# Performance work log

Measured on AMD Instinct MI355X. Metric: run time of the kernel, lower is better.

The kernel has to match this reference:

```python
import jax, jax.numpy as jnp
import numpy as np

N, C_IN, HF, WF = 4, 256, 128, 128
IMG_H, IMG_W = 1024, 1024
A = 3  # anchors per location (1 size x 3 aspect ratios), matches RPNHead
OBJ_THR, IOU_THR = 0.3, 0.7
PRE_NMS, POST_NMS = 2000, 300  # pre-NMS top-k (== top_k_proposals_training), post-NMS top-k (testing)


def setup_inputs() -> dict:
    key = jax.random.key(0)
    ks = jax.random.split(key, 5)
    return {
        "feat": jax.random.normal(ks[0], (N, C_IN, HF, WF), jnp.float32),
        "conv_w": jax.random.normal(ks[1], (256, C_IN, 3, 3), jnp.float32) * 0.02,
        "conv_b": jnp.zeros((256,), jnp.float32),
        "det_w": jax.random.normal(ks[2], (A, 256, 1, 1), jnp.float32) * 0.05,
        "det_b": jnp.zeros((A,), jnp.float32),
        "reg_w": jax.random.normal(ks[3], (4 * A, 256, 1, 1), jnp.float32) * 0.02,
        "reg_b": jnp.zeros((4 * A,), jnp.float32),
    }


def _conv(x, w, b, pad):
    y = jax.lax.conv_general_dilated(x, w, (1, 1), [(pad, pad), (pad, pad)],
                                     dimension_numbers=("NCHW", "OIHW", "NCHW"))
    return y + b[None, :, None, None]


def _anchors():
    # AnchorGenerator.generate_anchors + grid_anchors, stride = image // grid
    scales = jnp.array([128.0], jnp.float32)
    ratios = jnp.array([0.5, 1.0, 2.0], jnp.float32)
    hr = jnp.sqrt(ratios)
    wr = 1.0 / hr
    ws = (wr[:, None] * scales[None, :]).reshape(-1)
    hs = (hr[:, None] * scales[None, :]).reshape(-1)
    base = jnp.round(jnp.stack([-ws, -hs, ws, hs], axis=1) / 2.0)  # [A,4]
    sx = jnp.arange(WF, dtype=jnp.float32) * (IMG_W // WF)
    sy = jnp.arange(HF, dtype=jnp.float32) * (IMG_H // HF)
    yy, xx = jnp.meshgrid(sy, sx, indexing="ij")
    shifts = jnp.stack([xx.ravel(), yy.ravel(), xx.ravel(), yy.ravel()], axis=1)  # [H*W,4]
    return (shifts[:, None, :] + base[None, :, :]).reshape(-1, 4)  # [H*W*A,4]


def _decode(anchors, deltas):
    # Faithful to source, including the x/y swap in the anchor-center computation.
    x1, y1, x2, y2 = anchors[..., 0], anchors[..., 1], anchors[..., 2], anchors[..., 3]
    aw = x2 - x1
    ah = y2 - y1
    acx = y1 + aw / 2  # (sic) matches original code
    acy = x1 + ah / 2  # (sic)
    dx, dy, dw, dh = deltas[..., 0], deltas[..., 1], deltas[..., 2], deltas[..., 3]
    px = acx + dx * aw
    py = acy + dy * ah
    pw = aw * jnp.exp(dw)
    ph = ah * jnp.exp(dh)
    return jnp.stack([px - pw / 2, py - ph / 2, px + pw / 2, py + ph / 2], axis=-1)


def _filter_one(boxes, scores):
    # clip -> degenerate filter -> objectness threshold -> NMS -> top-k, fixed shapes
    w = boxes[:, 2] - boxes[:, 0]
    h = boxes[:, 3] - boxes[:, 1]
    valid = (scores > OBJ_THR) & (w > 0) & (h > 0)
    s = jnp.where(valid, scores, -jnp.inf)
    top_s, top_i = jax.lax.top_k(s, PRE_NMS)
    b = boxes[top_i]
    v = valid[top_i]
    area = jnp.maximum(b[:, 2] - b[:, 0], 0) * jnp.maximum(b[:, 3] - b[:, 1], 0)
    ix1 = jnp.maximum(b[:, None, 0], b[None, :, 0])
    iy1 = jnp.maximum(b[:, None, 1], b[None, :, 1])
    ix2 = jnp.minimum(b[:, None, 2], b[None, :, 2])
    iy2 = jnp.minimum(b[:, None, 3], b[None, :, 3])
    inter = jnp.maximum(ix2 - ix1, 0) * jnp.maximum(iy2 - iy1, 0)
    iou = inter / jnp.maximum(area[:, None] + area[None, :] - inter, 1e-9)
    idxs = jnp.arange(PRE_NMS)

    def body(keep, i):
        sup = jnp.any((iou[i] > IOU_THR) & keep & (idxs < i))
        return keep.at[i].set(v[i] & ~sup), None

    keep, _ = jax.lax.scan(body, jnp.zeros(PRE_NMS, bool), idxs)
    fs = jnp.where(keep, top_s, -jnp.inf)
    sel_s, sel_i = jax.lax.top_k(fs, POST_NMS)
    kept = keep[sel_i]
    out = jnp.concatenate([b[sel_i], sel_s[:, None]], axis=-1)  # [POST,5] = box + score
    return jnp.where(kept[:, None], out, 0.0)


def reference(feat, conv_w, conv_b, det_w, det_b, reg_w, reg_b):
    x = _conv(feat, conv_w, conv_b, 1)                      # fpn conv 3x3, no activation
    obj = jax.nn.sigmoid(_conv(x, det_w, det_b, 0)).reshape(N, -1)  # [N, A*H*W]
    d = _conv(x, reg_w, reg_b, 0)                           # [N, 4A, H, W]
    d = d.reshape(N, 4, A, HF, WF).transpose(0, 2, 3, 4, 1).reshape(N, -1, 4)
    anchors = _anchors()                                    # [A_total, 4]
    props = _decode(anchors[None], d)
    props = jnp.stack([
        jnp.clip(props[..., 0], 0, IMG_W), jnp.clip(props[..., 1], 0, IMG_H),
        jnp.clip(props[..., 2], 0, IMG_W), jnp.clip(props[..., 3], 0, IMG_H)], axis=-1)
    return jax.vmap(_filter_one)(props, obj)  # [N, POST_NMS, 5]
```

## Files before the change

kernel.cpp:

```cpp
#include <hip/hip_runtime.h>
#include <hip/hip_bf16.h>
#include <hip/hip_fp16.h>
#include <stdint.h>
#include <math.h>

#define N_IMG 4
#define CIN 256
#define HFD 128
#define WFD 128
#define HW (HFD*WFD)
#define NA 3
#define NPROP (NA*HW)
#define PRE_NMS 2000
#define POST_NMS 300

__device__ __forceinline__ unsigned long long rl64(unsigned long long v, int i) {
    unsigned int lo = (unsigned int)__builtin_amdgcn_readlane((int)(unsigned int)v, i);
    unsigned int hi = (unsigned int)__builtin_amdgcn_readlane((int)(unsigned int)(v >> 32), i);
    return ((unsigned long long)hi << 32) | (unsigned long long)lo;
}

__device__ __forceinline__ double sum4(const double* __restrict__ PART, size_t cp) {
    const size_t S = (size_t)1 << 20;
    return (PART[cp] + PART[cp + S]) + (PART[cp + 2 * S] + PART[cp + 3 * S]);
}

__device__ __forceinline__ void decode_box(int i, double dx, double dy, double dwv, double dhv,
                                           double& c1o, double& c2o, double& c3o, double& c4o) {
    int loc = i / 3, aa = i % 3;
    int hh = loc >> 7, wwi = loc & 127;
    double sx = (double)(wwi * 8), sy = (double)(hh * 8);
    double bx1 = (aa == 0) ? -91.0 : (aa == 1 ? -64.0 : -45.0);
    double by1 = (aa == 0) ? -45.0 : (aa == 1 ? -64.0 : -91.0);
    double x1 = sx + bx1, y1 = sy + by1, x2 = sx - bx1, y2 = sy - by1;
    double aw = x2 - x1, ahh = y2 - y1;
    double acx = y1 + aw * 0.5;
    double acy = x1 + ahh * 0.5;
    double px = acx + dx * aw, py = acy + dy * ahh;
    double pw = aw * exp(dwv), ph = ahh * exp(dhv);
    double c1 = px - pw * 0.5, c2 = py - ph * 0.5, c3 = px + pw * 0.5, c4 = py + ph * 0.5;
    c1o = fmin(fmax(c1, 0.0), 1024.0);
    c2o = fmin(fmax(c2, 0.0), 1024.0);
    c3o = fmin(fmax(c3, 0.0), 1024.0);
    c4o = fmin(fmax(c4, 0.0), 1024.0);
}

__global__ __launch_bounds__(256) void k_effw64(const float* __restrict__ cw, const float* __restrict__ cb,
                                                const float* __restrict__ dw_, const float* __restrict__ db_,
                                                const float* __restrict__ rw_, const float* __restrict__ rb_,
                                                double* __restrict__ E64, double* __restrict__ EB64,
                                                unsigned long long* __restrict__ PSPREF,
                                                int* __restrict__ PSNEED,
                                                uint32_t* __restrict__ HIST,
                                                uint32_t* __restrict__ CNT)
{
    int b = blockIdx.x;
    int tid = threadIdx.x;
    if (b < 144) {
        __shared__ float hwl[15][260];
        __shared__ float wt[256][16];
        int k0 = b * 16;
        for (int idx = tid; idx < 15 * 256; idx += 256) {
            int c = idx >> 8, co = idx & 255;
            hwl[c][co] = (c < 3) ? dw_[c * 256 + co] : rw_[(c - 3) * 256 + co];
        }
        for (int idx = tid; idx < 4096; idx += 256) {
            int co = idx >> 4, kk = idx & 15;
            wt[co][kk] = cw[co * 2304 + k0 + kk];
        }
        __syncthreads();
        int kk = tid >> 4, c = tid & 15;
        double s = 0.0;
        if (c < 15) {
#pragma unroll 4
            for (int co = 0; co < 256; co++) s += (double)hwl[c][co] * (double)wt[co][kk];
        }
        E64[(k0 + kk) * 16 + c] = s;
    } else {
        if (tid < 16) {
            int c = tid;
            double s = 0.0; double hb = 0.0;
            if (c < 15) {
                const float* hw = (c < 3) ? (dw_ + c * 256) : (rw_ + (c - 3) * 256);
                for (int co = 0; co < 256; co++) s += (double)hw[co] * (double)cb[co];
                hb = (double)((c < 3) ? db_[c] : rb_[c - 3]);
            }
            EB64[c] = s + hb;
        }
        for (int i = tid; i < N_IMG * 2048; i += 256) HIST[i] = 0u;
        if (tid < N_IMG) { PSPREF[tid] = 0ull; PSNEED[tid] = PRE_NMS; CNT[tid] = 0u; }
    }
}

__global__ __launch_bounds__(256, 7) void k_conv64(const float* __restrict__ feat,
                                                   const double* __restrict__ E64,
                                                   double* __restrict__ PART)
{
    __shared__ float in_t[8][3][132];
    __shared__ double wl[8][9][16];
    int b = blockIdx.x;
    int chunk = b & 3; int h = (b >> 2) & 127; int n = b >> 9;
    int tid = threadIdx.x;
    int q = tid & 63, g = tid >> 6;
    int w0 = q * 2;
    double acc[4][2];
#pragma unroll
    for (int cc = 0; cc < 4; cc++) { acc[cc][0] = 0.0; acc[cc][1] = 0.0; }

    for (int sl = 0; sl < 8; sl++) {
        int ci0 = (chunk << 6) + sl * 8;
        for (int idx = tid; idx < 8 * 396; idx += 256) {
            int ci = idx / 396; int rem = idx % 396; int dr = rem / 132; int dw = rem % 132;
            int gh = h - 1 + dr, gw = dw - 1;
            float v = 0.f;
            if (gh >= 0 && gh < HFD && gw >= 0 && gw < WFD)
                v = feat[(((n << 8) + ci0 + ci) << 14) + (gh << 7) + gw];
            in_t[ci][dr][dw] = v;
        }
        for (int idx = tid; idx < 1152; idx += 256) {
            ((double*)wl)[idx] = E64[(size_t)ci0 * 144 + idx];
        }
        __syncthreads();
        for (int ci = 0; ci < 8; ci++) {
#pragma unroll
            for (int r = 0; r < 3; r++) {
                float2 g0 = *(const float2*)&in_t[ci][r][w0];
                float2 g1 = *(const float2*)&in_t[ci][r][w0 + 2];
                float f[4] = {g0.x, g0.y, g1.x, g1.y};
#pragma unroll
                for (int s = 0; s < 3; s++) {
                    const double* wp = &wl[ci][r * 3 + s][g * 4];
                    double2 wv0 = *(const double2*)(wp);
                    double2 wv1 = *(const double2*)(wp + 2);
                    double pa = (double)f[s], pb = (double)f[s + 1];
                    acc[0][0] += wv0.x * pa; acc[0][1] += wv0.x * pb;
                    acc[1][0] += wv0.y * pa; acc[1][1] += wv0.y * pb;
                    acc[2][0] += wv1.x * pa; acc[2][1] += wv1.x * pb;
                    acc[3][0] += wv1.y * pa; acc[3][1] += wv1.y * pb;
                }
            }
        }
        __syncthreads();
    }
    int gpos = (n << 14) + (h << 7) + w0;
    double* base = PART + ((size_t)chunk << 20) + gpos;
#pragma unroll
    for (int cc = 0; cc < 4; cc++) {
        int c = g * 4 + cc;
        if (c < 15) {
            double2 st; st.x = acc[cc][0]; st.y = acc[cc][1];
            *(double2*)(base + (size_t)c * 65536) = st;
        }
    }
}

__global__ __launch_bounds__(256) void k_findecode(const double* __restrict__ PART,
                                                   const double* __restrict__ EB64,
                                                   unsigned long long* __restrict__ KEY64,
                                                   uint32_t* __restrict__ HIST)
{
    __shared__ uint32_t h2[2048];
    int tid = threadIdx.x;
    for (int i = tid; i < 2048; i += 256) h2[i] = 0u;
    __syncthreads();
    int p = blockIdx.x * 256 + tid;
    int n = p >> 14, pos = p & 16383;
    double L[15];
#pragma unroll
    for (int c = 0; c < 15; c++)
        L[c] = sum4(PART, (size_t)c * 65536 + p) + EB64[c];
#pragma unroll
    for (int a = 0; a < 3; a++) {
        double logit = L[a];
        double score = 1.0 / (1.0 + exp(-logit));
        int i = a * HW + pos;
        double c1, c2, c3, c4;
        decode_box(i, L[3 + a], L[6 + a], L[9 + a], L[12 + a], c1, c2, c3, c4);
        bool valid = (score > 0.3) && (c3 - c1 > 0.0) && (c4 - c2 > 0.0);
        unsigned long long key = valid ? ~((unsigned long long)__double_as_longlong(score)) : ~0ull;
        KEY64[(size_t)n * NPROP + i] = key;
        atomicAdd(&h2[(uint32_t)(key >> 53)], 1u);
    }
    __syncthreads();
    uint32_t* G = HIST + n * 2048;
    for (int i = tid; i < 2048; i += 256) {
        uint32_t v = h2[i];
        if (v) atomicAdd(&G[i], v);
    }
}

__global__ __launch_bounds__(256) void k_hist(const unsigned long long* __restrict__ KEY64,
                                              const unsigned long long* __restrict__ PSPREF,
                                              uint32_t* __restrict__ HIST, int L)
{
    __shared__ uint32_t h[2048];
    int blk = blockIdx.x; int n = blk >> 4, sub = blk & 15;
    int tid = threadIdx.x;
    for (int i = tid; i < 2048; i += 256) h[i] = 0u;
    __syncthreads();
    int sh = 53 - 11 * L;
    unsigned long long pref = PSPREF[n];
    const unsigned long long* K = KEY64 + (size_t)n * NPROP + sub * 3072;
    for (int i = tid; i < 3072; i += 256) {
        unsigned long long k = K[i];
        bool in = (L == 0) || ((k >> (sh + 11)) == pref);
        if (in) atomicAdd(&h[(uint32_t)((k >> sh) & 2047ull)], 1u);
    }
    __syncthreads();
    uint32_t* G = HIST + n * 2048;
    for (int i = tid; i < 2048; i += 256) {
        uint32_t v = h[i];
        if (v) atomicAdd(&G[i], v);
    }
}

__global__ __launch_bounds__(256) void k_pick(uint32_t* __restrict__ HIST,
                                              unsigned long long* __restrict__ PSPREF,
                                              int* __restrict__ PSNEED)
{
    int n = blockIdx.x; int tid = threadIdx.x;
    __shared__ uint32_t hl[2048];
    __shared__ uint32_t psum[256];
    uint32_t* G = HIST + n * 2048;
    for (int i = tid; i < 2048; i += 256) hl[i] = G[i];
    __syncthreads();
    {
        uint32_t s = 0;
        for (int qq = 0; qq < 8; qq++) s += hl[tid * 8 + qq];
        psum[tid] = s;
    }
    __syncthreads();
    if (tid == 0) {
        int need = PSNEED[n];
        unsigned long long pref = PSPREF[n];
        uint32_t cum = 0; int g = 255;
        for (int t = 0; t < 256; t++) { uint32_t c = psum[t]; if (cum + c >= (uint32_t)need) { g = t; break; } cum += c; }
        int bsel = g * 8 + 7;
        for (int t = g * 8; t < g * 8 + 8; t++) { uint32_t c = hl[t]; if (cum + c >= (uint32_t)need) { bsel = t; break; } cum += c; }
        PSNEED[n] = need - (int)cum;
        PSPREF[n] = (pref << 11) | (unsigned long long)bsel;
    }
    __syncthreads();
    for (int i = tid; i < 2048; i += 256) G[i] = 0u;
}

__global__ __launch_bounds__(256) void k_collect(const unsigned long long* __restrict__ KEY64,
                                                 const unsigned long long* __restrict__ PSPREF,
                                                 uint32_t* __restrict__ CNT,
                                                 unsigned long long* __restrict__ CANDK,
                                                 uint32_t* __restrict__ CANDI)
{
    int blk = blockIdx.x; int n = blk >> 4, sub = blk & 15;
    int tid = threadIdx.x;
    unsigned long long pref44 = PSPREF[n];
    const unsigned long long* K = KEY64 + (size_t)n * NPROP;
    int base = sub * 3072;
    for (int i = tid; i < 3072; i += 256) {
        unsigned long long k = K[base + i];
        if (k != ~0ull && (k >> 20) <= pref44) {
            uint32_t p2 = atomicAdd(&CNT[n], 1u);
            if (p2 < 2048u) { CANDK[n * 2048 + p2] = k; CANDI[n * 2048 + p2] = (uint32_t)(base + i); }
        }
    }
}

__global__ __launch_bounds__(1024) void k_finalsel(const uint32_t* __restrict__ CNT,
                                                   const unsigned long long* __restrict__ CANDK,
                                                   const uint32_t* __restrict__ CANDI,
                                                   const double* __restrict__ PART,
                                                   const double* __restrict__ EB64,
                                                   unsigned long long* __restrict__ skeys,
                                                   double* __restrict__ bsort,
                                                   double* __restrict__ area)
{
    int n = blockIdx.x; int tid = threadIdx.x;
    __shared__ unsigned long long selk[2048];
    __shared__ uint32_t seli[2048];
    uint32_t cnt = CNT[n]; if (cnt > 2048u) cnt = 2048u;
    for (int t = tid; t < 2048; t += 1024) {
        if (t < (int)cnt) { selk[t] = CANDK[n * 2048 + t]; seli[t] = CANDI[n * 2048 + t]; }
        else { selk[t] = ~0ull; seli[t] = 0xFFFFFFFFu; }
    }
    __syncthreads();
    for (unsigned k2 = 2; k2 <= 2048; k2 <<= 1) {
        for (unsigned jx = k2 >> 1; jx > 0; jx >>= 1) {
            for (int t = tid; t < 2048; t += 1024) {
                unsigned ixj = (unsigned)t ^ jx;
                if (ixj > (unsigned)t) {
                    bool up = ((t & k2) == 0);
                    unsigned long long ka = selk[t], kb = selk[ixj];
                    uint32_t ia = seli[t], ib = seli[ixj];
                    bool agt = (ka > kb) || (ka == kb && ia > ib);
                    if (up ? agt : !agt) {
                        selk[t] = kb; selk[ixj] = ka;
                        seli[t] = ib; seli[ixj] = ia;
                    }
                }
            }
            __syncthreads();
        }
    }
    for (int t = tid; t < 2048; t += 1024) {
        bool valid = (t < PRE_NMS) && (selk[t] != ~0ull);
        if (t < PRE_NMS) skeys[(size_t)n * PRE_NMS + t] = valid ? selk[t] : ~0ull;
        double b0 = 0, b1 = 0, b2 = 0, b3 = 0;
        if (valid) {
            int i = (int)seli[t];
            int a = i >> 14, pos = i & 16383;
            size_t p = ((size_t)n << 14) + pos;
            double dx  = sum4(PART, (size_t)(3 + a)  * 65536 + p) + EB64[3 + a];
            double dy  = sum4(PART, (size_t)(6 + a)  * 65536 + p) + EB64[6 + a];
            double dwv = sum4(PART, (size_t)(9 + a)  * 65536 + p) + EB64[9 + a];
            double dhv = sum4(PART, (size_t)(12 + a) * 65536 + p) + EB64[12 + a];
            decode_box(i, dx, dy, dwv, dhv, b0, b1, b2, b3);
        }
        double* bs = bsort + (((size_t)(n * 2048 + t)) << 2);
        bs[0] = b0; bs[1] = b1; bs[2] = b2; bs[3] = b3;
        area[(size_t)n * 2048 + t] = fmax(b2 - b0, 0.0) * fmax(b3 - b1, 0.0);
    }
}

__global__ __launch_bounds__(256) void k_iou2(const double* __restrict__ bsort,
                                              const double* __restrict__ area,
                                              unsigned long long* __restrict__ mat)
{
    int blk = blockIdx.x; int n = blk >> 6; int rt = blk & 63;
    int tid = threadIdx.x;
    int r = tid >> 3, g = tid & 7;
    int i = rt * 32 + r;
    const double* bp = bsort + ((size_t)n * 2048 + i) * 4;
    double bx0 = bp[0], bx1_ = bp[1], bx2_ = bp[2], bx3 = bp[3];
    double ai = area[(size_t)n * 2048 + i];
    __shared__ double cbx[512][4];
    __shared__ double ca[512];
    for (int cc = 0; cc < 4; cc++) {
        if ((cc + 1) * 512 <= rt * 32) continue;
        __syncthreads();
        for (int idx = tid; idx < 512; idx += 256) {
            const double* sp = bsort + ((size_t)n * 2048 + cc * 512 + idx) * 4;
            cbx[idx][0] = sp[0]; cbx[idx][1] = sp[1]; cbx[idx][2] = sp[2]; cbx[idx][3] = sp[3];
            ca[idx] = area[(size_t)n * 2048 + cc * 512 + idx];
        }
        __syncthreads();
        unsigned long long wd = 0ull;
        for (int jb = 0; jb < 64; jb++) {
            int jr = (jb + g * 9) & 63;
            int jj = g * 64 + jr;
            double ix1 = fmax(bx0, cbx[jj][0]);
            double iy1 = fmax(bx1_, cbx[jj][1]);
            double ix2 = fmin(bx2_, cbx[jj][2]);
            double iy2 = fmin(bx3, cbx[jj][3]);
            double inter = fmax(ix2 - ix1, 0.0) * fmax(iy2 - iy1, 0.0);
            double den = fmax(ai + ca[jj] - inter, 1e-9);
            double iou = inter / den;
            if (iou > 0.7) wd |= (1ull << jr);
        }
        mat[((size_t)n * 2048 + i) * 32 + cc * 8 + g] = wd;
    }
}

__global__ __launch_bounds__(256) void k_nms3(const unsigned long long* __restrict__ skeys,
                                              const double* __restrict__ bsort,
                                              const unsigned long long* __restrict__ mat,
                                              float* __restrict__ out)
{
    int n = blockIdx.x; int tid = threadIdx.x;
    int lane = tid & 63;
    __shared__ unsigned long long rb[2][64][33];
    __shared__ unsigned long long sup_lds[32];
    __shared__ unsigned long long vb[32];
    __shared__ unsigned long long kbw[32];
    __shared__ int s_stop;
    float* dout = out + n * (POST_NMS * 5);
    for (int t = tid; t < POST_NMS * 5; t += 256) dout[t] = 0.f;
    if (tid < 32) { sup_lds[tid] = 0ull; kbw[tid] = 0ull; }
    if (tid == 0) s_stop = 0;
    if (tid < 64) {
        for (int i0 = 0; i0 < 2048; i0 += 64) {
            int i = i0 + lane;
            unsigned long long k = (i < PRE_NMS) ? skeys[(size_t)n * PRE_NMS + i] : ~0ull;
            unsigned long long m = __ballot(k != ~0ull);
            if (lane == 0) vb[i0 >> 6] = m;
        }
    }
    int r = tid >> 2, w0 = (tid & 3) * 8;
    {
        const unsigned long long* src = mat + ((size_t)n * 2048 + r) * 32 + w0;
        ulonglong2 a = *(const ulonglong2*)(src);
        ulonglong2 b = *(const ulonglong2*)(src + 2);
        ulonglong2 c2 = *(const ulonglong2*)(src + 4);
        ulonglong2 d = *(const ulonglong2*)(src + 6);
        unsigned long long* dst = &rb[0][r][w0];
        dst[0] = a.x; dst[1] = a.y; dst[2] = b.x; dst[3] = b.y;
        dst[4] = c2.x; dst[5] = c2.y; dst[6] = d.x; dst[7] = d.y;
    }
    __syncthreads();
    int total_kept = 0;
    for (int c = 0; c < 32; c++) {
        if (s_stop) break;
        int cur = c & 1, nxt = cur ^ 1;
        ulonglong2 pa, pb, pc, pd;
        bool pf = (c + 1 < 32);
        if (pf) {
            const unsigned long long* src = mat + ((size_t)n * 2048 + (c + 1) * 64 + r) * 32 + w0;
            pa = *(const ulonglong2*)(src);
            pb = *(const ulonglong2*)(src + 2);
            pc = *(const ulonglong2*)(src + 4);
            pd = *(const ulonglong2*)(src + 6);
        }
        if (tid < 64) {
            unsigned long long M = rb[cur][lane][c];
            unsigned long long supw = sup_lds[c];
            unsigned long long vbw = vb[c];
            unsigned long long km = 0ull;
#pragma unroll
            for (int ii = 0; ii < 64; ii++) {
                unsigned long long bit = 1ull << ii;
                if ((vbw & bit) && !(supw & bit)) {
                    km |= bit;
                    supw |= rl64(M, ii);
                }
            }
            if (lane == 0) {
                kbw[c] = km;
                total_kept += __popcll(km);
                if (total_kept >= POST_NMS) s_stop = 1;
            }
        }
        __syncthreads();
        {
            int w = tid & 31, g = tid >> 5;
            unsigned long long km2 = kbw[c];
            unsigned long long sub = (km2 >> (g * 8)) & 0xFFull;
            unsigned long long acc = 0ull;
            while (sub) {
                int bpos = __ffsll((long long)sub) - 1;
                sub &= sub - 1;
                acc |= rb[cur][g * 8 + bpos][w];
            }
            if (acc) atomicOr(&sup_lds[w], acc);
        }
        if (pf) {
            unsigned long long* dst = &rb[nxt][r][w0];
            dst[0] = pa.x; dst[1] = pa.y; dst[2] = pb.x; dst[3] = pb.y;
            dst[4] = pc.x; dst[5] = pc.y; dst[6] = pd.x; dst[7] = pd.y;
        }
        __syncthreads();
    }
    if (tid < 64) {
        int running = 0;
        for (int i0 = 0; i0 < 2048; i0 += 64) {
            int i = i0 + lane;
            bool kp = (i < PRE_NMS) && ((kbw[i >> 6] >> (i & 63)) & 1ull);
            unsigned long long m = __ballot(kp);
            if (kp) {
                int rk = running + __popcll(m & ((1ull << lane) - 1ull));
                if (rk < POST_NMS) {
                    const double* bp2 = bsort + ((size_t)n * 2048 + i) * 4;
                    unsigned long long k = skeys[(size_t)n * PRE_NMS + i];
                    double s = __longlong_as_double((long long)~k);
                    float* o = dout + rk * 5;
                    o[0] = (float)bp2[0]; o[1] = (float)bp2[1];
                    o[2] = (float)bp2[2]; o[3] = (float)bp2[3];
                    o[4] = (float)s;
                }
            }
            running += __popcll(m);
        }
    }
}

extern "C" void kernel_launch(void* const* d_in, const int* in_sizes, int n_in,
                              void* d_out, int out_size, void* d_ws, size_t ws_size,
                              hipStream_t stream) {
    (void)in_sizes; (void)n_in; (void)out_size; (void)ws_size;
    const float* feat   = (const float*)d_in[0];
    const float* conv_w = (const float*)d_in[1];
    const float* conv_b = (const float*)d_in[2];
    const float* det_w  = (const float*)d_in[3];
    const float* det_b  = (const float*)d_in[4];
    const float* reg_w  = (const float*)d_in[5];
    const float* reg_b  = (const float*)d_in[6];
    float* out = (float*)d_out;

    char* w = (char*)d_ws;
    double* E64 = (double*)w;                          w += (size_t)2304 * 16 * 8;
    double* EB64 = (double*)w;                         w += 128;
    double* PART = (double*)w;                         w += (size_t)4 << 23;
    unsigned long long* KEY64 = (unsigned long long*)w; w += (size_t)N_IMG * NPROP * 8;
    unsigned long long* PSPREF = (unsigned long long*)w; w += N_IMG * 8;
    int* PSNEED = (int*)w;                             w += 64;
    uint32_t* HIST = (uint32_t*)w;                     w += (size_t)N_IMG * 2048 * 4;
    uint32_t* CNT = (uint32_t*)w;                      w += 64;
    unsigned long long* CANDK = (unsigned long long*)w; w += (size_t)N_IMG * 2048 * 8;
    uint32_t* CANDI = (uint32_t*)w;                    w += (size_t)N_IMG * 2048 * 4;
    unsigned long long* SKEY = (unsigned long long*)w; w += (size_t)N_IMG * PRE_NMS * 8;
    double* BSORT = (double*)w;                        w += (size_t)N_IMG * 2048 * 4 * 8;
    double* AREA = (double*)w;                         w += (size_t)N_IMG * 2048 * 8;
    unsigned long long* MAT = (unsigned long long*)w;  w += (size_t)N_IMG * 2048 * 32 * 8;

    k_effw64<<<dim3(145), dim3(256), 0, stream>>>(conv_w, conv_b, det_w, det_b, reg_w, reg_b,
                                                  E64, EB64, PSPREF, PSNEED, HIST, CNT);
    k_conv64<<<dim3(2048), dim3(256), 0, stream>>>(feat, E64, PART);
    k_findecode<<<dim3(256), dim3(256), 0, stream>>>(PART, EB64, KEY64, HIST);
    k_pick<<<dim3(N_IMG), dim3(256), 0, stream>>>(HIST, PSPREF, PSNEED);
    for (int L = 1; L < 4; L++) {
        k_hist<<<dim3(64), dim3(256), 0, stream>>>(KEY64, PSPREF, HIST, L);
        k_pick<<<dim3(N_IMG), dim3(256), 0, stream>>>(HIST, PSPREF, PSNEED);
    }
    k_collect<<<dim3(64), dim3(256), 0, stream>>>(KEY64, PSPREF, CNT, CANDK, CANDI);
    k_finalsel<<<dim3(N_IMG), dim3(1024), 0, stream>>>(CNT, CANDK, CANDI, PART, EB64, SKEY, BSORT, AREA);
    k_iou2<<<dim3(N_IMG * 64), dim3(256), 0, stream>>>(BSORT, AREA, MAT);
    k_nms3<<<dim3(N_IMG), dim3(256), 0, stream>>>(SKEY, BSORT, MAT, out);
}
```

Baseline: 416.6 us.

## Process two output rows per block in fused conv with 4-pixel register tiles

The fused 3x3 conv kernel now computes two output rows per block, with each thread holding four horizontal pixels by four channels instead of two pixels. This halves the grid, loads a 4-row input halo so the input tile serves two rows, and converts the int-to-float input loads to float4 vectorized loads with explicit zero padding of the edge columns. Register pressure rises (16 double accumulators plus 6 staged inputs), so launch bounds drop from 7 to 4 blocks per CU. Overlapping rows across the grid now reuse the halo, but there are fewer blocks to hide latency.

```diff
diff --git a/kernel.cpp b/kernel.cpp
--- a/kernel.cpp
+++ b/kernel.cpp
@@ -92,30 +92,41 @@
     }
 }
 
-__global__ __launch_bounds__(256, 7) void k_conv64(const float* __restrict__ feat,
+__global__ __launch_bounds__(256, 4) void k_conv64(const float* __restrict__ feat,
                                                    const double* __restrict__ E64,
                                                    double* __restrict__ PART)
 {
-    __shared__ float in_t[8][3][132];
+    __shared__ float in_t[8][4][132];
     __shared__ double wl[8][9][16];
     int b = blockIdx.x;
-    int chunk = b & 3; int h = (b >> 2) & 127; int n = b >> 9;
+    int chunk = b & 3; int hp = (b >> 2) & 63; int n = b >> 8;
+    int h0 = hp * 2;
     int tid = threadIdx.x;
-    int q = tid & 63, g = tid >> 6;
-    int w0 = q * 2;
-    double acc[4][2];
-#pragma unroll
-    for (int cc = 0; cc < 4; cc++) { acc[cc][0] = 0.0; acc[cc][1] = 0.0; }
+    int q = tid & 63;
+    int row = q >> 5, qq = q & 31, w0 = qq * 4;
+    int g = tid >> 6;
+    double acc[4][4];
+#pragma unroll
+    for (int cc = 0; cc < 4; cc++)
+#pragma unroll
+        for (int px = 0; px < 4; px++) acc[cc][px] = 0.0;
 
     for (int sl = 0; sl < 8; sl++) {
         int ci0 = (chunk << 6) + sl * 8;
-        for (int idx = tid; idx < 8 * 396; idx += 256) {
-            int ci = idx / 396; int rem = idx % 396; int dr = rem / 132; int dw = rem % 132;
-            int gh = h - 1 + dr, gw = dw - 1;
-            float v = 0.f;
-            if (gh >= 0 && gh < HFD && gw >= 0 && gw < WFD)
-                v = feat[(((n << 8) + ci0 + ci) << 14) + (gh << 7) + gw];
-            in_t[ci][dr][dw] = v;
+        for (int t = tid; t < 1024; t += 256) {
+            int seg = t & 31;
+            int rid = t >> 5;
+            int ci = rid >> 2, dr = rid & 3;
+            int gh = h0 - 1 + dr;
+            float4 v = make_float4(0.f, 0.f, 0.f, 0.f);
+            if (gh >= 0 && gh < HFD)
+                v = *(const float4*)&feat[(((size_t)((n << 8) + ci0 + ci)) << 14) + (gh << 7) + (seg << 2)];
+            float* d = &in_t[ci][dr][1 + (seg << 2)];
+            d[0] = v.x; d[1] = v.y; d[2] = v.z; d[3] = v.w;
+        }
+        if (tid < 128) {
+            int ci = tid >> 4, r2 = tid & 15, dr = r2 >> 2, col = r2 & 3;
+            if (col < 3) in_t[ci][dr][col == 0 ? 0 : 128 + col] = 0.f;
         }
         for (int idx = tid; idx < 1152; idx += 256) {
             ((double*)wl)[idx] = E64[(size_t)ci0 * 144 + idx];
@@ -124,32 +135,42 @@
         for (int ci = 0; ci < 8; ci++) {
 #pragma unroll
             for (int r = 0; r < 3; r++) {
-                float2 g0 = *(const float2*)&in_t[ci][r][w0];
-                float2 g1 = *(const float2*)&in_t[ci][r][w0 + 2];
-                float f[4] = {g0.x, g0.y, g1.x, g1.y};
+                const float* rp = &in_t[ci][row + r][w0];
+                float2 a0 = *(const float2*)(rp);
+                float2 a1 = *(const float2*)(rp + 2);
+                float2 a2 = *(const float2*)(rp + 4);
+                double fv[6];
+                fv[0] = (double)a0.x; fv[1] = (double)a0.y;
+                fv[2] = (double)a1.x; fv[3] = (double)a1.y;
+                fv[4] = (double)a2.x; fv[5] = (double)a2.y;
 #pragma unroll
                 for (int s = 0; s < 3; s++) {
                     const double* wp = &wl[ci][r * 3 + s][g * 4];
                     double2 wv0 = *(const double2*)(wp);
                     double2 wv1 = *(const double2*)(wp + 2);
-                    double pa = (double)f[s], pb = (double)f[s + 1];
-                    acc[0][0] += wv0.x * pa; acc[0][1] += wv0.x * pb;
-                    acc[1][0] += wv0.y * pa; acc[1][1] += wv0.y * pb;
-                    acc[2][0] += wv1.x * pa; acc[2][1] += wv1.x * pb;
-                    acc[3][0] += wv1.y * pa; acc[3][1] += wv1.y * pb;
+#pragma unroll
+                    for (int px = 0; px < 4; px++) {
+                        double f = fv[s + px];
+                        acc[0][px] += wv0.x * f;
+                        acc[1][px] += wv0.y * f;
+                        acc[2][px] += wv1.x * f;
+                        acc[3][px] += wv1.y * f;
+                    }
                 }
             }
         }
         __syncthreads();
     }
-    int gpos = (n << 14) + (h << 7) + w0;
+    int gpos = (n << 14) + ((h0 + row) << 7) + w0;
     double* base = PART + ((size_t)chunk << 20) + gpos;
 #pragma unroll
     for (int cc = 0; cc < 4; cc++) {
         int c = g * 4 + cc;
         if (c < 15) {
-            double2 st; st.x = acc[cc][0]; st.y = acc[cc][1];
-            *(double2*)(base + (size_t)c * 65536) = st;
+            double2 s0; s0.x = acc[cc][0]; s0.y = acc[cc][1];
+            double2 s1; s1.x = acc[cc][2]; s1.y = acc[cc][3];
+            *(double2*)(base + (size_t)c * 65536) = s0;
+            *(double2*)(base + (size_t)c * 65536 + 2) = s1;
         }
     }
 }
@@ -501,7 +522,7 @@
 
     k_effw64<<<dim3(145), dim3(256), 0, stream>>>(conv_w, conv_b, det_w, det_b, reg_w, reg_b,
                                                   E64, EB64, PSPREF, PSNEED, HIST, CNT);
-    k_conv64<<<dim3(2048), dim3(256), 0, stream>>>(feat, E64, PART);
+    k_conv64<<<dim3(1024), dim3(256), 0, stream>>>(feat, E64, PART);
     k_findecode<<<dim3(256), dim3(256), 0, stream>>>(PART, EB64, KEY64, HIST);
     k_pick<<<dim3(N_IMG), dim3(256), 0, stream>>>(HIST, PSPREF, PSNEED);
     for (int L = 1; L < 4; L++) {
```

After: 374.5 us. -10.1%, faster.
